# Kernel optimization log

Measured on AMD Instinct MI355X. Metric: run time of the kernel, lower is better.

## Reference

```python
import jax, jax.numpy as jnp
import numpy as np

NUM_SEGMENTS = 128  # num_total_segments


def setup_inputs() -> dict:
    key = jax.random.key(0)
    k1, k2 = jax.random.split(key)
    B, C, Hp, Wp = 2, 768, 28, 28
    Hi, Wi = 392, 392
    F_semantic_patches = jax.random.normal(k1, (B, C, Hp, Wp), dtype=jnp.float32)
    segmentation_mask = jax.random.randint(k2, (B, Hi, Wi), 0, NUM_SEGMENTS, dtype=jnp.int64)
    return {"F_semantic_patches": F_semantic_patches, "segmentation_mask": segmentation_mask}


def reference(F_semantic_patches, segmentation_mask):
    S = NUM_SEGMENTS
    B, C, Hp, Wp = F_semantic_patches.shape
    _, Hi, Wi = segmentation_mask.shape

    # F.interpolate(mode='nearest') to (Hp, Wp): src index = floor(dst * in/out)
    ih = (jnp.arange(Hp) * Hi) // Hp  # [Hp]
    iw = (jnp.arange(Wp) * Wi) // Wp  # [Wp]
    seg_feat = segmentation_mask[:, ih[:, None], iw[None, :]]  # [B,Hp,Wp] int

    # flatten features to [B*Hp*Wp, C] (permute 0,2,3,1 then reshape)
    flat_feat = jnp.transpose(F_semantic_patches, (0, 2, 3, 1)).reshape(-1, C)
    batch_idx = jnp.arange(B, dtype=seg_feat.dtype)[:, None, None]
    gid = (batch_idx * S + jnp.clip(seg_feat, 0, S - 1)).reshape(-1)  # [B*Hp*Wp]

    # scatter_mean over global segment ids, dim_size = B*S
    sums = jax.ops.segment_sum(flat_feat, gid, num_segments=B * S)  # [B*S, C]
    counts = jax.ops.segment_sum(jnp.ones_like(gid, dtype=flat_feat.dtype), gid,
                                 num_segments=B * S)  # [B*S]
    cnt = counts[:, None]
    # mean with nan_to_num(nan=0.0): empty segments -> 0
    seg_avg = jnp.where(cnt > 0, sums / jnp.maximum(cnt, 1), jnp.zeros_like(sums))

    # gather back at full pixel resolution
    pid = (batch_idx * S + jnp.clip(segmentation_mask, 0, S - 1)).reshape(-1)  # [B*Hi*Wi]
    painted = seg_avg[pid].reshape(B, Hi, Wi, C)  # [B,Hi,Wi,C]
    return jnp.transpose(painted, (0, 3, 1, 2))  # [B,C,Hi,Wi]
```

## Files before the change

kernel.cpp:

```cpp
#include <hip/hip_runtime.h>

#define NSEG 128
#define BB 2
#define CC 768
#define CC4 (CC/4)
#define HP 28
#define WP 28
#define HI 392
#define WI 392
#define NPIX (HI*WI)
#define NPIX4 (NPIX/4)
#define CPB4 16

typedef float f32x4 __attribute__((ext_vector_type(4)));

__global__ void pid_kernel(const int* __restrict__ mask, unsigned int* __restrict__ sb) {
    int g = blockIdx.x * blockDim.x + threadIdx.x;
    if (g >= BB * NPIX4) return;
    int4 m = ((const int4*)mask)[g];
    unsigned int s0 = (unsigned int)min(max(m.x, 0), NSEG - 1);
    unsigned int s1 = (unsigned int)min(max(m.y, 0), NSEG - 1);
    unsigned int s2 = (unsigned int)min(max(m.z, 0), NSEG - 1);
    unsigned int s3 = (unsigned int)min(max(m.w, 0), NSEG - 1);
    sb[g] = s0 | (s1 << 8) | (s2 << 16) | (s3 << 24);
}

__global__ void accum_kernel(const float* __restrict__ F, const int* __restrict__ mask,
                             float* __restrict__ sums, float* __restrict__ counts) {
    int cell = blockIdx.x;
    int b = cell / (HP * WP);
    int rem = cell - b * (HP * WP);
    int hp = rem / WP;
    int wp = rem - hp * WP;
    int m = mask[(size_t)b * NPIX + (hp * 14) * WI + (wp * 14)];
    int s = min(max(m, 0), NSEG - 1);
    for (int c = threadIdx.x; c < CC; c += blockDim.x) {
        float v = F[((b * CC + c) * HP + hp) * WP + wp];
        atomicAdd(&sums[(size_t)(b * CC + c) * NSEG + s], v);
    }
    if (threadIdx.x == 0) atomicAdd(&counts[b * NSEG + s], 1.0f);
}

__global__ __launch_bounds__(128) void div_kernel(float* __restrict__ sums,
                                                  const float* __restrict__ counts) {
    int quad = blockIdx.x;
    int b = quad / CC4;
    int s = threadIdx.x;
    float* base = sums + ((size_t)quad << 9);
    float cnt = counts[b * NSEG + s];
    float v0 = base[s];
    float v1 = base[s + NSEG];
    float v2 = base[s + 2 * NSEG];
    float v3 = base[s + 3 * NSEG];
    float inv = (cnt > 0.0f) ? (1.0f / cnt) : 0.0f;
    __syncthreads();
    ((f32x4*)base)[s] = (f32x4){v0 * inv, v1 * inv, v2 * inv, v3 * inv};
}

__global__ __launch_bounds__(256) void paint_kernel(const f32x4* __restrict__ avg4,
                                                    const unsigned int* __restrict__ sb,
                                                    float* __restrict__ out) {
    int b = blockIdx.z;
    int g = blockIdx.x * blockDim.x + threadIdx.x;
    if (g >= NPIX4) return;
    unsigned int packed = sb[(size_t)b * NPIX4 + g];
    int s0 = packed & 255;
    int s1 = (packed >> 8) & 255;
    int s2 = (packed >> 16) & 255;
    int s3 = (packed >> 24) & 255;
    int q0 = blockIdx.y * CPB4;
    const f32x4* tbl = avg4 + ((size_t)(b * CC4 + q0) << 7);
    f32x4* outp = (f32x4*)out + (size_t)(b * CC + 4 * q0) * NPIX4 + g;
    #pragma unroll 4
    for (int i = 0; i < CPB4; ++i) {
        const f32x4* t = tbl + ((size_t)i << 7);
        f32x4 a = t[s0], bb = t[s1], c = t[s2], d = t[s3];
        #pragma unroll
        for (int j = 0; j < 4; ++j) {
            f32x4 v = {a[j], bb[j], c[j], d[j]};
            __builtin_nontemporal_store(v, outp + (size_t)(4 * i + j) * NPIX4);
        }
    }
}

extern "C" void kernel_launch(void* const* d_in, const int* in_sizes, int n_in,
                              void* d_out, int out_size, void* d_ws, size_t ws_size,
                              hipStream_t stream) {
    const float* F = (const float*)d_in[0];
    const int* mask = (const int*)d_in[1];
    float* out = (float*)d_out;

    float* sums = (float*)d_ws;
    float* counts = sums + BB * CC * NSEG;
    unsigned int* sb = (unsigned int*)(counts + BB * NSEG);

    (void)hipMemsetAsync(d_ws, 0, (size_t)(BB * CC * NSEG + BB * NSEG) * sizeof(float), stream);

    int ngroups = BB * NPIX4;
    pid_kernel<<<(ngroups + 255) / 256, 256, 0, stream>>>(mask, sb);
    accum_kernel<<<BB * HP * WP, 256, 0, stream>>>(F, mask, sums, counts);
    div_kernel<<<BB * CC4, 128, 0, stream>>>(sums, counts);
    paint_kernel<<<dim3((NPIX4 + 255) / 256, CC4 / CPB4, BB), 256, 0, stream>>>(
        (const f32x4*)sums, sb, out);
}
```

Baseline: 989.3 us.

## Stage per-channel-quad average table in LDS and loop pixels per block

The paint kernel now gives each block one channel quad and one batch. It copies that quad's 128-entry segment-average table into shared memory, then loops over a span of pixels, looking up averages from LDS instead of global/L2 gathers. The aim is to replace scattered global table reads with LDS lookups. In exchange, the packed segment ids are re-read once per channel quad (192 times instead of 12), and the grid changes to 8 pixel spans × 192 quads × 2 batches.

New measurement: 1.049 ms. +6.1%, slower.

```diff
diff --git a/kernel.cpp b/kernel.cpp
--- a/kernel.cpp
+++ b/kernel.cpp
@@ -10,7 +10,8 @@
 #define WI 392
 #define NPIX (HI*WI)
 #define NPIX4 (NPIX/4)
-#define CPB4 16
+#define NXBLK 8
+#define XSPAN (NPIX4/NXBLK)
 
 typedef float f32x4 __attribute__((ext_vector_type(4)));
 
@@ -60,25 +61,26 @@
 __global__ __launch_bounds__(256) void paint_kernel(const f32x4* __restrict__ avg4,
                                                     const unsigned int* __restrict__ sb,
                                                     float* __restrict__ out) {
+    __shared__ f32x4 tbl[NSEG];
+    int q = blockIdx.y;
     int b = blockIdx.z;
-    int g = blockIdx.x * blockDim.x + threadIdx.x;
-    if (g >= NPIX4) return;
-    unsigned int packed = sb[(size_t)b * NPIX4 + g];
-    int s0 = packed & 255;
-    int s1 = (packed >> 8) & 255;
-    int s2 = (packed >> 16) & 255;
-    int s3 = (packed >> 24) & 255;
-    int q0 = blockIdx.y * CPB4;
-    const f32x4* tbl = avg4 + ((size_t)(b * CC4 + q0) << 7);
-    f32x4* outp = (f32x4*)out + (size_t)(b * CC + 4 * q0) * NPIX4 + g;
-    #pragma unroll 4
-    for (int i = 0; i < CPB4; ++i) {
-        const f32x4* t = tbl + ((size_t)i << 7);
-        f32x4 a = t[s0], bb = t[s1], c = t[s2], d = t[s3];
+    if (threadIdx.x < NSEG)
+        tbl[threadIdx.x] = avg4[(((size_t)(b * CC4 + q)) << 7) + threadIdx.x];
+    __syncthreads();
+
+    const unsigned int* sbp = sb + (size_t)b * NPIX4;
+    f32x4* outp = (f32x4*)out + (size_t)(b * CC + 4 * q) * NPIX4;
+    int gend = (blockIdx.x + 1) * XSPAN;
+    for (int g = blockIdx.x * XSPAN + threadIdx.x; g < gend; g += 256) {
+        unsigned int packed = sbp[g];
+        f32x4 a = tbl[packed & 255];
+        f32x4 bb = tbl[(packed >> 8) & 255];
+        f32x4 c = tbl[(packed >> 16) & 255];
+        f32x4 d = tbl[(packed >> 24) & 255];
         #pragma unroll
         for (int j = 0; j < 4; ++j) {
             f32x4 v = {a[j], bb[j], c[j], d[j]};
-            __builtin_nontemporal_store(v, outp + (size_t)(4 * i + j) * NPIX4);
+            __builtin_nontemporal_store(v, outp + (size_t)j * NPIX4 + g);
         }
     }
 }
@@ -100,6 +102,6 @@
     pid_kernel<<<(ngroups + 255) / 256, 256, 0, stream>>>(mask, sb);
     accum_kernel<<<BB * HP * WP, 256, 0, stream>>>(F, mask, sums, counts);
     div_kernel<<<BB * CC4, 128, 0, stream>>>(sums, counts);
-    paint_kernel<<<dim3((NPIX4 + 255) / 256, CC4 / CPB4, BB), 256, 0, stream>>>(
+    paint_kernel<<<dim3(NXBLK, CC4, BB), 256, 0, stream>>>(
         (const f32x4*)sums, sb, out);
 }
```
